# Kernel tuning notes

Measured on AMD Instinct MI355X. Metric: run time of the kernel, lower is better.

The kernel has to match this reference:

```python
import jax, jax.numpy as jnp
import numpy as np

GAMMAS = jnp.array([2.7, 2.1, 2.4, 2.0, 3.0, 2.9, 3.0, 2.5, 2.1, 2.6, 2.0, 2.1, 2.7, 2.4, 2.2], dtype=jnp.float32)

B, NCLS, H, W = 32, 15, 256, 256
K, CREG = 500, 2


def setup_inputs() -> dict:
    key = jax.random.key(0)
    ks = jax.random.split(key, 6)
    pred = jax.random.uniform(ks[0], (B, NCLS, H, W), dtype=jnp.float32)
    gt = jax.random.uniform(ks[1], (B, NCLS, H, W), dtype=jnp.float32)
    output = jax.random.normal(ks[2], (B, CREG, H, W), dtype=jnp.float32)
    mask = jax.random.randint(ks[3], (B, K), 0, 2, dtype=jnp.int32)
    ind = jax.random.randint(ks[4], (B, K), 0, H * W)
    target = jax.random.normal(ks[5], (B, K, CREG), dtype=jnp.float32)
    inde = jax.random.randint(jax.random.fold_in(key, 7), (B, K, 3), 0, 15)
    return {"pred": pred, "gt": gt, "output": output, "mask": mask,
            "ind": ind, "target": target, "inde": inde}


def _forward(pred, gt, output, mask, ind, target, inde):
    b, c_out = output.shape[0], output.shape[1]
    k = ind.shape[1]
    # _tranpose_and_gather_feat: [B,C,H,W] -> [B,HW,C], gather along dim 1
    feat = jnp.transpose(output, (0, 2, 3, 1)).reshape(b, -1, c_out)
    pre = jnp.take_along_axis(feat, ind[:, :, None].astype(jnp.int32), axis=1)  # [B,K,C]

    d = pre - target
    ad = jnp.abs(d)
    huber = jnp.where(ad < 1.0, 0.5 * d * d, ad - 0.5)
    l_bk = huber.mean(axis=2)  # [B,K]

    pos_mask = mask.astype(bool)
    factor = jnp.arctan(l_bk) * (2.0 / jnp.pi)
    vals = jnp.where(pos_mask, factor, 1.0).reshape(-1)

    b_idx = jnp.broadcast_to(jnp.arange(b)[:, None], (b, k)).reshape(-1)
    ch = inde[..., 0].reshape(-1)
    yy = inde[..., 1].reshape(-1)
    xx = inde[..., 2].reshape(-1)
    # in-place multiplicative scatter; torch's pred_uni aliases pred so the
    # modified tensor is used for BOTH pred_cat and pred_cat_uni below
    pred_mod = pred.at[b_idx, ch, yy, xx].multiply(vals)

    # loss is overwritten each loop iteration in the original: only the LAST
    # positive's smooth-L1 loss survives (0 if no positives)
    flat_m = pos_mask.reshape(-1)
    flat_l = l_bk.reshape(-1)
    last = jnp.max(jnp.where(flat_m, jnp.arange(flat_m.shape[0]), -1))
    loss0 = jnp.where(last >= 0, flat_l[jnp.clip(last, 0)], 0.0)

    # focal term, vectorized over the 15 class channels
    eps = 1e-12
    g = GAMMAS[None, :, None, None]
    pos_inds = (gt == 1.0).astype(pred.dtype)
    neg_inds = (gt < 1.0).astype(pred.dtype)
    neg_weights = jnp.power(1.0 - gt, 4)
    pos_loss = jnp.log(pred_mod + eps) * jnp.power(1.0 - pred_mod, g) * pos_inds
    neg_loss = jnp.log(1.0 - pred_mod + eps) * jnp.power(pred_mod, g) * neg_weights * neg_inds
    per_ch = jnp.sum(pos_loss + neg_loss, axis=(0, 2, 3))  # [15]
    loss = loss0 - jnp.sum(per_ch * GAMMAS * 0.5)

    num_pos = pos_inds.sum()
    return jnp.where(num_pos == 0, loss, loss / num_pos)


def reference(pred, gt, output, mask, ind, target, inde):
    return _forward(pred, gt, output, mask, ind, target, inde)
```

## Files before the change

### kernel.cpp

```cpp
#include <hip/hip_runtime.h>
#include <math.h>

#define BB 32
#define NCLS 15
#define HH 256
#define WW 256
#define KK 500
#define HW (HH*WW)
#define NELEM (BB*NCLS*HW)
#define N4 (NELEM/4)
#define NM (BB*NCLS*16*16)
#define BK (BB*KK)

#define FG 1920
#define FT 256
#define SLAB4 16384
#define QUART 4096
#define BKPB 9

typedef float v4f __attribute__((ext_vector_type(4)));

#define OFF_LBK 4
#define OFF_M   16384

__constant__ float c_gammas[15] = {2.7f,2.1f,2.4f,2.0f,3.0f,2.9f,3.0f,2.5f,
                                   2.1f,2.6f,2.0f,2.1f,2.7f,2.4f,2.2f};

#define EXP2F(x) __builtin_amdgcn_exp2f(x)
#define LOG2F(x) __builtin_amdgcn_logf(x)
#define LN2 0.69314718055994530942f

__device__ __forceinline__ float elem(float p, float g, float gam, float& np) {
    float t    = 1.0f - g;
    float t2   = t * t;
    float negw = (g < 1.0f) ? t2 * t2 : 0.0f;
    float pw   = EXP2F(gam * LOG2F(p));
    float v    = (LN2 * LOG2F(1.0f - p + 1e-12f)) * pw * negw;
    if (g == 1.0f) {
        np += 1.0f;
        v += (LN2 * LOG2F(p + 1e-12f)) * EXP2F(gam * LOG2F(1.0f - p));
    }
    return v;
}

__device__ __forceinline__ float elem4(v4f p, v4f g, float gam, float& np) {
    return elem(p.x, g.x, gam, np) + elem(p.y, g.y, gam, np)
         + elem(p.z, g.z, gam, np) + elem(p.w, g.w, gam, np);
}

__device__ __forceinline__ float blockReduceSum(float v) {
    __shared__ float sh[4];
    #pragma unroll
    for (int o = 32; o > 0; o >>= 1) v += __shfl_down(v, o);
    int lane = threadIdx.x & 63, w = threadIdx.x >> 6;
    if (lane == 0) sh[w] = v;
    __syncthreads();
    float r = 0.0f;
    if (threadIdx.x == 0) r = sh[0] + sh[1] + sh[2] + sh[3];
    __syncthreads();
    return r;
}

__global__ __launch_bounds__(256) void k_init(float* ws) {
    int i = blockIdx.x * blockDim.x + threadIdx.x;
    if (i == 0) {
        ws[0] = 0.0f;
        ws[1] = 0.0f;
        ((int*)ws)[2] = -1;
        ((int*)ws)[3] = 0;
    }
    if (i < NM) ws[OFF_M + i] = 1.0f;
}

__global__ __launch_bounds__(256) void k_fused(const v4f*   __restrict__ pred,
                                               const v4f*   __restrict__ gt,
                                               const float* __restrict__ output,
                                               const int*   __restrict__ mask,
                                               const int*   __restrict__ ind,
                                               const float* __restrict__ target,
                                               const int*   __restrict__ inde,
                                               float* ws) {
    const int tid = threadIdx.x;
    const int blk = blockIdx.x;

    int lastv = -1;
    if (tid < BKPB) {
        int t = blk * BKPB + tid;
        if (t < BK) {
            int b = t / KK;
            int pos = ind[t];
            const float* ob = output + (size_t)b * 2 * HW;
            float p0 = ob[pos];
            float p1 = ob[HW + pos];
            float d0 = p0 - target[t*2 + 0];
            float d1 = p1 - target[t*2 + 1];
            float a0 = fabsf(d0), a1 = fabsf(d1);
            float h0 = (a0 < 1.0f) ? 0.5f*d0*d0 : a0 - 0.5f;
            float h1 = (a1 < 1.0f) ? 0.5f*d1*d1 : a1 - 0.5f;
            float l  = 0.5f * (h0 + h1);
            ws[OFF_LBK + t] = l;
            if (mask[t] != 0) {
                lastv = t;
                float factor = atanf(l) * 0.63661977236758134308f;
                int ch = inde[t*3 + 0];
                int yy = inde[t*3 + 1];
                int xx = inde[t*3 + 2];
                int mi = ((b*NCLS + ch)*16 + yy)*16 + xx;
                unsigned int* addr = (unsigned int*)(ws + OFF_M + mi);
                unsigned int old = *addr, assumed;
                do {
                    assumed = old;
                    float nv = __uint_as_float(assumed) * factor;
                    old = atomicCAS(addr, assumed, __float_as_uint(nv));
                } while (old != assumed);
            }
        }
    }
    #pragma unroll
    for (int o = 8; o > 0; o >>= 1) lastv = max(lastv, __shfl_down(lastv, o));
    if (tid == 0 && lastv >= 0) atomicMax(((int*)ws) + 2, lastv);

    const int slab = blk >> 2;
    const int c    = slab % NCLS;
    const float gam = c_gammas[c];
    const int base = slab * SLAB4 + (blk & 3) * QUART + tid;

    float acc = 0.0f, np = 0.0f;
    #pragma unroll 1
    for (int k = 0; k < 4; ++k) {
        int i0 = base + k * 1024;
        v4f p0 = __builtin_nontemporal_load(pred + i0);
        v4f g0 = __builtin_nontemporal_load(gt   + i0);
        v4f p1 = __builtin_nontemporal_load(pred + i0 + 256);
        v4f g1 = __builtin_nontemporal_load(gt   + i0 + 256);
        v4f p2 = __builtin_nontemporal_load(pred + i0 + 512);
        v4f g2 = __builtin_nontemporal_load(gt   + i0 + 512);
        v4f p3 = __builtin_nontemporal_load(pred + i0 + 768);
        v4f g3 = __builtin_nontemporal_load(gt   + i0 + 768);
        acc += elem4(p0, g0, gam, np);
        acc += elem4(p1, g1, gam, np);
        acc += elem4(p2, g2, gam, np);
        acc += elem4(p3, g3, gam, np);
    }
    acc *= gam;

    float bs = blockReduceSum(acc);
    if (tid == 0 && bs != 0.0f) atomicAdd(&ws[0], bs);
    float bn = blockReduceSum(np);
    if (tid == 0 && bn != 0.0f) atomicAdd(&ws[1], bn);
}

__global__ __launch_bounds__(256) void k_corr(const float* __restrict__ pred,
                                              const float* __restrict__ gt,
                                              float* ws, float* out) {
    int i = blockIdx.x * blockDim.x + threadIdx.x;
    float acc = 0.0f, dummy = 0.0f;
    float m = ws[OFF_M + i];
    if (m != 1.0f) {
        int x  = i & 15;
        int y  = (i >> 4) & 15;
        int bc = i >> 8;
        int c  = bc % NCLS;
        size_t off = ((size_t)bc << 16) + (size_t)(y * WW + x);
        float p = pred[off];
        float g = gt[off];
        float gam = c_gammas[c];
        acc = gam * (elem(p * m, g, gam, dummy) - elem(p, g, gam, dummy));
    }
    float bs = blockReduceSum(acc);
    if (threadIdx.x == 0) {
        if (bs != 0.0f) atomicAdd(&ws[0], bs);
        __threadfence();
        int done = atomicAdd(((int*)ws) + 3, 1);
        if (done == gridDim.x - 1) {
            float S  = atomicAdd(&ws[0], 0.0f);
            float np = atomicAdd(&ws[1], 0.0f);
            int last = ((volatile int*)ws)[2];
            float loss0 = (last >= 0) ? ws[OFF_LBK + last] : 0.0f;
            float loss = loss0 - 0.5f * S;
            out[0] = (np == 0.0f) ? loss : loss / np;
        }
    }
}

extern "C" void kernel_launch(void* const* d_in, const int* in_sizes, int n_in,
                              void* d_out, int out_size, void* d_ws, size_t ws_size,
                              hipStream_t stream) {
    const float* pred   = (const float*)d_in[0];
    const float* gt     = (const float*)d_in[1];
    const float* output = (const float*)d_in[2];
    const int*   mask   = (const int*)d_in[3];
    const int*   ind    = (const int*)d_in[4];
    const float* target = (const float*)d_in[5];
    const int*   inde   = (const int*)d_in[6];
    float* ws  = (float*)d_ws;
    float* out = (float*)d_out;

    k_init <<<(NM + 255)/256, 256, 0, stream>>>(ws);
    k_fused<<<FG, FT, 0, stream>>>((const v4f*)pred, (const v4f*)gt,
                                   output, mask, ind, target, inde, ws);
    k_corr <<<NM/256, 256, 0, stream>>>(pred, gt, ws, out);
}
```

Before: 294.4 us.

## Fuse init, focal sum, and scatter correction into a single kernel

Merges the three kernels into one launch. 32 extra blocks, one per batch item, do the regression gather, a multiplicative scatter into a shared-memory multiplier table, and the correction term for modified pixels. The remaining blocks stream pred and gt to compute the focal sum. The last-positive loss is packed with its index into a 64-bit atomicMax, and the global accumulators live in device globals that the finishing block resets. This removes two launches and the workspace round trips, at the cost of 32 slow auxiliary blocks and persistent global state.

```diff
diff --git a/kernel.cpp b/kernel.cpp
--- a/kernel.cpp
+++ b/kernel.cpp
@@ -9,19 +9,15 @@
 #define HW (HH*WW)
 #define NELEM (BB*NCLS*HW)
 #define N4 (NELEM/4)
-#define NM (BB*NCLS*16*16)
-#define BK (BB*KK)
-
-#define FG 1920
+#define NSLOT (NCLS*16*16)
+
+#define AUXB 32
+#define FG (AUXB + 1920)
 #define FT 256
 #define SLAB4 16384
 #define QUART 4096
-#define BKPB 9
 
 typedef float v4f __attribute__((ext_vector_type(4)));
-
-#define OFF_LBK 4
-#define OFF_M   16384
 
 __constant__ float c_gammas[15] = {2.7f,2.1f,2.4f,2.0f,3.0f,2.9f,3.0f,2.5f,
                                    2.1f,2.6f,2.0f,2.1f,2.7f,2.4f,2.2f};
@@ -29,6 +25,11 @@
 #define EXP2F(x) __builtin_amdgcn_exp2f(x)
 #define LOG2F(x) __builtin_amdgcn_logf(x)
 #define LN2 0.69314718055994530942f
+
+__device__ float g_S = 0.0f;
+__device__ float g_np = 0.0f;
+__device__ unsigned long long g_lastpack = 0ULL;
+__device__ unsigned int g_count = 0u;
 
 __device__ __forceinline__ float elem(float p, float g, float gam, float& np) {
     float t    = 1.0f - g;
@@ -61,33 +62,32 @@
     return r;
 }
 
-__global__ __launch_bounds__(256) void k_init(float* ws) {
-    int i = blockIdx.x * blockDim.x + threadIdx.x;
-    if (i == 0) {
-        ws[0] = 0.0f;
-        ws[1] = 0.0f;
-        ((int*)ws)[2] = -1;
-        ((int*)ws)[3] = 0;
-    }
-    if (i < NM) ws[OFF_M + i] = 1.0f;
-}
-
-__global__ __launch_bounds__(256) void k_fused(const v4f*   __restrict__ pred,
-                                               const v4f*   __restrict__ gt,
-                                               const float* __restrict__ output,
-                                               const int*   __restrict__ mask,
-                                               const int*   __restrict__ ind,
-                                               const float* __restrict__ target,
-                                               const int*   __restrict__ inde,
-                                               float* ws) {
+__global__ __launch_bounds__(256) void k_mega(const v4f*   __restrict__ pred4,
+                                              const v4f*   __restrict__ gt4,
+                                              const float* __restrict__ pred,
+                                              const float* __restrict__ gt,
+                                              const float* __restrict__ output,
+                                              const int*   __restrict__ mask,
+                                              const int*   __restrict__ ind,
+                                              const float* __restrict__ target,
+                                              const int*   __restrict__ inde,
+                                              float* out) {
+    __shared__ float shM[NSLOT];
+    __shared__ unsigned long long shL[4];
     const int tid = threadIdx.x;
     const int blk = blockIdx.x;
 
-    int lastv = -1;
-    if (tid < BKPB) {
-        int t = blk * BKPB + tid;
-        if (t < BK) {
-            int b = t / KK;
+    float acc = 0.0f;
+    float np  = 0.0f;
+
+    if (blk < AUXB) {
+        const int b = blk;
+        for (int i = tid; i < NSLOT; i += FT) shM[i] = 1.0f;
+        __syncthreads();
+
+        unsigned long long lp = 0ULL;
+        for (int k = tid; k < KK; k += FT) {
+            int t = b * KK + k;
             int pos = ind[t];
             const float* ob = output + (size_t)b * 2 * HW;
             float p0 = ob[pos];
@@ -98,15 +98,17 @@
             float h0 = (a0 < 1.0f) ? 0.5f*d0*d0 : a0 - 0.5f;
             float h1 = (a1 < 1.0f) ? 0.5f*d1*d1 : a1 - 0.5f;
             float l  = 0.5f * (h0 + h1);
-            ws[OFF_LBK + t] = l;
             if (mask[t] != 0) {
-                lastv = t;
+                unsigned long long pk =
+                    ((unsigned long long)(unsigned)(t + 1) << 32) |
+                    (unsigned long long)__float_as_uint(l);
+                lp = (pk > lp) ? pk : lp;
                 float factor = atanf(l) * 0.63661977236758134308f;
                 int ch = inde[t*3 + 0];
                 int yy = inde[t*3 + 1];
                 int xx = inde[t*3 + 2];
-                int mi = ((b*NCLS + ch)*16 + yy)*16 + xx;
-                unsigned int* addr = (unsigned int*)(ws + OFF_M + mi);
+                int mi = (ch*16 + yy)*16 + xx;
+                unsigned int* addr = (unsigned int*)&shM[mi];
                 unsigned int old = *addr, assumed;
                 do {
                     assumed = old;
@@ -115,70 +117,81 @@
                 } while (old != assumed);
             }
         }
+        #pragma unroll
+        for (int o = 32; o > 0; o >>= 1) {
+            unsigned long long other = __shfl_down(lp, o);
+            lp = (other > lp) ? other : lp;
+        }
+        int lane = tid & 63, w = tid >> 6;
+        if (lane == 0) shL[w] = lp;
+        __syncthreads();
+        if (tid == 0) {
+            unsigned long long m0 = shL[0] > shL[1] ? shL[0] : shL[1];
+            unsigned long long m1 = shL[2] > shL[3] ? shL[2] : shL[3];
+            unsigned long long mm = m0 > m1 ? m0 : m1;
+            if (mm) atomicMax(&g_lastpack, mm);
+        }
+        __syncthreads();
+
+        for (int i = tid; i < NSLOT; i += FT) {
+            float m = shM[i];
+            if (m != 1.0f) {
+                int ch = i >> 8;
+                int yy = (i >> 4) & 15;
+                int xx = i & 15;
+                size_t off = ((size_t)(b*NCLS + ch) << 16) + (yy*WW + xx);
+                float p = pred[off];
+                float g = gt[off];
+                float gam = c_gammas[ch];
+                float dmy = 0.0f;
+                acc += gam * (elem(p*m, g, gam, dmy) - elem(p, g, gam, dmy));
+            }
+        }
+    } else {
+        const int sblk = blk - AUXB;
+        const int slab = sblk >> 2;
+        const int c    = slab % NCLS;
+        const float gam = c_gammas[c];
+        const int base = slab * SLAB4 + (sblk & 3) * QUART + tid;
+
+        float sacc = 0.0f;
+        #pragma unroll 1
+        for (int k = 0; k < 4; ++k) {
+            int i0 = base + k * 1024;
+            v4f p0 = __builtin_nontemporal_load(pred4 + i0);
+            v4f g0 = __builtin_nontemporal_load(gt4   + i0);
+            v4f p1 = __builtin_nontemporal_load(pred4 + i0 + 256);
+            v4f g1 = __builtin_nontemporal_load(gt4   + i0 + 256);
+            v4f p2 = __builtin_nontemporal_load(pred4 + i0 + 512);
+            v4f g2 = __builtin_nontemporal_load(gt4   + i0 + 512);
+            v4f p3 = __builtin_nontemporal_load(pred4 + i0 + 768);
+            v4f g3 = __builtin_nontemporal_load(gt4   + i0 + 768);
+            sacc += elem4(p0, g0, gam, np);
+            sacc += elem4(p1, g1, gam, np);
+            sacc += elem4(p2, g2, gam, np);
+            sacc += elem4(p3, g3, gam, np);
+        }
+        acc = gam * sacc;
     }
-    #pragma unroll
-    for (int o = 8; o > 0; o >>= 1) lastv = max(lastv, __shfl_down(lastv, o));
-    if (tid == 0 && lastv >= 0) atomicMax(((int*)ws) + 2, lastv);
-
-    const int slab = blk >> 2;
-    const int c    = slab % NCLS;
-    const float gam = c_gammas[c];
-    const int base = slab * SLAB4 + (blk & 3) * QUART + tid;
-
-    float acc = 0.0f, np = 0.0f;
-    #pragma unroll 1
-    for (int k = 0; k < 4; ++k) {
-        int i0 = base + k * 1024;
-        v4f p0 = __builtin_nontemporal_load(pred + i0);
-        v4f g0 = __builtin_nontemporal_load(gt   + i0);
-        v4f p1 = __builtin_nontemporal_load(pred + i0 + 256);
-        v4f g1 = __builtin_nontemporal_load(gt   + i0 + 256);
-        v4f p2 = __builtin_nontemporal_load(pred + i0 + 512);
-        v4f g2 = __builtin_nontemporal_load(gt   + i0 + 512);
-        v4f p3 = __builtin_nontemporal_load(pred + i0 + 768);
-        v4f g3 = __builtin_nontemporal_load(gt   + i0 + 768);
-        acc += elem4(p0, g0, gam, np);
-        acc += elem4(p1, g1, gam, np);
-        acc += elem4(p2, g2, gam, np);
-        acc += elem4(p3, g3, gam, np);
-    }
-    acc *= gam;
 
     float bs = blockReduceSum(acc);
-    if (tid == 0 && bs != 0.0f) atomicAdd(&ws[0], bs);
     float bn = blockReduceSum(np);
-    if (tid == 0 && bn != 0.0f) atomicAdd(&ws[1], bn);
-}
-
-__global__ __launch_bounds__(256) void k_corr(const float* __restrict__ pred,
-                                              const float* __restrict__ gt,
-                                              float* ws, float* out) {
-    int i = blockIdx.x * blockDim.x + threadIdx.x;
-    float acc = 0.0f, dummy = 0.0f;
-    float m = ws[OFF_M + i];
-    if (m != 1.0f) {
-        int x  = i & 15;
-        int y  = (i >> 4) & 15;
-        int bc = i >> 8;
-        int c  = bc % NCLS;
-        size_t off = ((size_t)bc << 16) + (size_t)(y * WW + x);
-        float p = pred[off];
-        float g = gt[off];
-        float gam = c_gammas[c];
-        acc = gam * (elem(p * m, g, gam, dummy) - elem(p, g, gam, dummy));
-    }
-    float bs = blockReduceSum(acc);
-    if (threadIdx.x == 0) {
-        if (bs != 0.0f) atomicAdd(&ws[0], bs);
+    if (tid == 0) {
+        if (bs != 0.0f) atomicAdd(&g_S, bs);
+        if (bn != 0.0f) atomicAdd(&g_np, bn);
         __threadfence();
-        int done = atomicAdd(((int*)ws) + 3, 1);
-        if (done == gridDim.x - 1) {
-            float S  = atomicAdd(&ws[0], 0.0f);
-            float np = atomicAdd(&ws[1], 0.0f);
-            int last = ((volatile int*)ws)[2];
-            float loss0 = (last >= 0) ? ws[OFF_LBK + last] : 0.0f;
+        unsigned int done = atomicAdd(&g_count, 1u);
+        if (done % FG == FG - 1) {
+            float S   = atomicAdd(&g_S, 0.0f);
+            float npv = atomicAdd(&g_np, 0.0f);
+            unsigned long long lpv = atomicAdd(&g_lastpack, 0ULL);
+            float loss0 = (lpv >> 32) ?
+                __uint_as_float((unsigned int)(lpv & 0xffffffffu)) : 0.0f;
             float loss = loss0 - 0.5f * S;
-            out[0] = (np == 0.0f) ? loss : loss / np;
+            out[0] = (npv == 0.0f) ? loss : loss / npv;
+            atomicExch(&g_S, 0.0f);
+            atomicExch(&g_np, 0.0f);
+            atomicExch(&g_lastpack, 0ULL);
         }
     }
 }
@@ -193,11 +206,10 @@
     const int*   ind    = (const int*)d_in[4];
     const float* target = (const float*)d_in[5];
     const int*   inde   = (const int*)d_in[6];
-    float* ws  = (float*)d_ws;
     float* out = (float*)d_out;
-
-    k_init <<<(NM + 255)/256, 256, 0, stream>>>(ws);
-    k_fused<<<FG, FT, 0, stream>>>((const v4f*)pred, (const v4f*)gt,
-                                   output, mask, ind, target, inde, ws);
-    k_corr <<<NM/256, 256, 0, stream>>>(pred, gt, ws, out);
-}
+    (void)d_ws; (void)ws_size;
+
+    k_mega<<<FG, FT, 0, stream>>>((const v4f*)pred, (const v4f*)gt,
+                                  pred, gt, output, mask, ind, target, inde,
+                                  out);
+}
```

Result: slower. 349.2 us (+18.6%).

## Halve grid and software-pipeline focal loads with double-buffered register sets

Applied to the files above, without the earlier changes.

Each block now covers half a class slab instead of a quarter, so the grid has half as many blocks and each block takes 17 regression entries instead of 9. The streaming loop is fully unrolled with two register buffers: the next chunk's loads are issued before the current chunk is computed, with sched_barriers to keep that order. The aim is more memory-level parallelism per wave to hide HBM latency. The cost is higher register use (launch bounds set to 4) and fewer blocks to spread across CUs.

```diff
diff --git a/kernel.cpp b/kernel.cpp
--- a/kernel.cpp
+++ b/kernel.cpp
@@ -12,11 +12,11 @@
 #define NM (BB*NCLS*16*16)
 #define BK (BB*KK)
 
-#define FG 1920
+#define FG 960
 #define FT 256
 #define SLAB4 16384
-#define QUART 4096
-#define BKPB 9
+#define HALF4 8192
+#define BKPB 17
 
 typedef float v4f __attribute__((ext_vector_type(4)));
 
@@ -72,14 +72,27 @@
     if (i < NM) ws[OFF_M + i] = 1.0f;
 }
 
-__global__ __launch_bounds__(256) void k_fused(const v4f*   __restrict__ pred,
-                                               const v4f*   __restrict__ gt,
-                                               const float* __restrict__ output,
-                                               const int*   __restrict__ mask,
-                                               const int*   __restrict__ ind,
-                                               const float* __restrict__ target,
-                                               const int*   __restrict__ inde,
-                                               float* ws) {
+#define NTL(p) __builtin_nontemporal_load(p)
+#define SB __builtin_amdgcn_sched_barrier(0);
+
+#define PREF(P,G,off) \
+    P##0 = NTL(pb + (off));       G##0 = NTL(gb + (off)); \
+    P##1 = NTL(pb + (off) + 256); G##1 = NTL(gb + (off) + 256); \
+    P##2 = NTL(pb + (off) + 512); G##2 = NTL(gb + (off) + 512); \
+    P##3 = NTL(pb + (off) + 768); G##3 = NTL(gb + (off) + 768);
+
+#define COMP(P,G) \
+    sacc += elem4(P##0, G##0, gam, np); sacc += elem4(P##1, G##1, gam, np); \
+    sacc += elem4(P##2, G##2, gam, np); sacc += elem4(P##3, G##3, gam, np);
+
+__global__ __launch_bounds__(256, 4) void k_fused(const v4f*   __restrict__ pred4,
+                                                  const v4f*   __restrict__ gt4,
+                                                  const float* __restrict__ output,
+                                                  const int*   __restrict__ mask,
+                                                  const int*   __restrict__ ind,
+                                                  const float* __restrict__ target,
+                                                  const int*   __restrict__ inde,
+                                                  float* ws) {
     const int tid = threadIdx.x;
     const int blk = blockIdx.x;
 
@@ -117,32 +130,30 @@
         }
     }
     #pragma unroll
-    for (int o = 8; o > 0; o >>= 1) lastv = max(lastv, __shfl_down(lastv, o));
+    for (int o = 16; o > 0; o >>= 1) lastv = max(lastv, __shfl_down(lastv, o));
     if (tid == 0 && lastv >= 0) atomicMax(((int*)ws) + 2, lastv);
 
-    const int slab = blk >> 2;
+    const int slab = blk >> 1;
     const int c    = slab % NCLS;
     const float gam = c_gammas[c];
-    const int base = slab * SLAB4 + (blk & 3) * QUART + tid;
-
-    float acc = 0.0f, np = 0.0f;
-    #pragma unroll 1
-    for (int k = 0; k < 4; ++k) {
-        int i0 = base + k * 1024;
-        v4f p0 = __builtin_nontemporal_load(pred + i0);
-        v4f g0 = __builtin_nontemporal_load(gt   + i0);
-        v4f p1 = __builtin_nontemporal_load(pred + i0 + 256);
-        v4f g1 = __builtin_nontemporal_load(gt   + i0 + 256);
-        v4f p2 = __builtin_nontemporal_load(pred + i0 + 512);
-        v4f g2 = __builtin_nontemporal_load(gt   + i0 + 512);
-        v4f p3 = __builtin_nontemporal_load(pred + i0 + 768);
-        v4f g3 = __builtin_nontemporal_load(gt   + i0 + 768);
-        acc += elem4(p0, g0, gam, np);
-        acc += elem4(p1, g1, gam, np);
-        acc += elem4(p2, g2, gam, np);
-        acc += elem4(p3, g3, gam, np);
-    }
-    acc *= gam;
+    const v4f* pb = pred4 + slab * SLAB4 + (blk & 1) * HALF4 + tid;
+    const v4f* gb = gt4   + slab * SLAB4 + (blk & 1) * HALF4 + tid;
+
+    float sacc = 0.0f, np = 0.0f;
+    v4f pA0, pA1, pA2, pA3, gA0, gA1, gA2, gA3;
+    v4f pB0, pB1, pB2, pB3, gB0, gB1, gB2, gB3;
+
+    PREF(pA, gA, 0)
+    PREF(pB, gB, 1024) SB COMP(pA, gA)
+    PREF(pA, gA, 2048) SB COMP(pB, gB)
+    PREF(pB, gB, 3072) SB COMP(pA, gA)
+    PREF(pA, gA, 4096) SB COMP(pB, gB)
+    PREF(pB, gB, 5120) SB COMP(pA, gA)
+    PREF(pA, gA, 6144) SB COMP(pB, gB)
+    PREF(pB, gB, 7168) SB COMP(pA, gA)
+    COMP(pB, gB)
+
+    float acc = gam * sacc;
 
     float bs = blockReduceSum(acc);
     if (tid == 0 && bs != 0.0f) atomicAdd(&ws[0], bs);
```

Result: slower. 325.0 us (+10.4%).
